# Performance work log

Hardware: AMD Instinct MI355X
Metric: run time of the kernel (lower is better)

The kernel has to match this reference:

```python
import jax, jax.numpy as jnp
import numpy as np

HIDDEN = 2048
HEADS = 16
KV_HEADS = 1
HEAD_DIM = 128
SEQ = 2048
BATCH = 1
LAM = 0.5


def _rotate_half(x):
    h = x.shape[-1] // 2
    return jnp.concatenate([-x[..., h:], x[..., :h]], axis=-1)


def _apply_rope(t, cos, sin):
    # t: [B,S,H,D], cos/sin: [S,D] -> broadcast over batch & heads
    c = cos[None, :, None, :]
    s = sin[None, :, None, :]
    return t * c + _rotate_half(t) * s


def setup_inputs() -> dict:
    key = jax.random.key(0)
    ks = jax.random.split(key, 8)
    x = jax.random.normal(ks[0], (BATCH, SEQ, HIDDEN), dtype=jnp.float32)
    # realistic RoPE tables, rotate-half layout: [S, D]
    inv_freq = 1.0 / (10000.0 ** (np.arange(0, HEAD_DIM, 2, dtype=np.float32) / HEAD_DIM))
    t = np.arange(SEQ, dtype=np.float32)
    ang = np.outer(t, inv_freq)                      # [S, D/2]
    ang = np.concatenate([ang, ang], axis=-1)        # [S, D]
    freqs_cos = jnp.asarray(np.cos(ang))
    freqs_sin = jnp.asarray(np.sin(ang))
    mask = jnp.tril(jnp.ones((SEQ, SEQ), dtype=bool))  # causal, True = attend
    scale = 1.0 / np.sqrt(HIDDEN)
    q1_w = jax.random.normal(ks[1], (HIDDEN, HEADS * HEAD_DIM), dtype=jnp.float32) * scale
    q2_w = jax.random.normal(ks[2], (HIDDEN, HEADS * HEAD_DIM), dtype=jnp.float32) * scale
    k_w = jax.random.normal(ks[3], (HIDDEN, KV_HEADS * HEAD_DIM), dtype=jnp.float32) * scale
    v_w = jax.random.normal(ks[4], (HIDDEN, KV_HEADS * HEAD_DIM), dtype=jnp.float32) * scale
    out_w = jax.random.normal(ks[5], (HEADS * HEAD_DIM, HIDDEN), dtype=jnp.float32) * scale
    return {"x": x, "freqs_cos": freqs_cos, "freqs_sin": freqs_sin, "mask": mask,
            "q1_w": q1_w, "q2_w": q2_w, "k_w": k_w, "v_w": v_w, "out_w": out_w}


def reference(x, freqs_cos, freqs_sin, mask, q1_w, q2_w, k_w, v_w, out_w):
    B, S, _ = x.shape
    q1 = (x @ q1_w).reshape(B, S, HEADS, HEAD_DIM)
    q2 = (x @ q2_w).reshape(B, S, HEADS, HEAD_DIM)
    k = (x @ k_w).reshape(B, S, KV_HEADS, HEAD_DIM)
    v = (x @ v_w).reshape(B, S, KV_HEADS, HEAD_DIM)
    q1 = _apply_rope(q1, freqs_cos, freqs_sin)
    q2 = _apply_rope(q2, freqs_cos, freqs_sin)
    k = _apply_rope(k, freqs_cos, freqs_sin)
    # MQA broadcast of the single KV head
    k = jnp.repeat(k, HEADS // KV_HEADS, axis=2)  # [B,S,H,D]
    v = jnp.repeat(v, HEADS // KV_HEADS, axis=2)
    inv_sqrt_d = 1.0 / jnp.sqrt(jnp.float32(HEAD_DIM))
    s1 = jnp.einsum('bqhd,bkhd->bhqk', q1, k) * inv_sqrt_d
    s2 = jnp.einsum('bqhd,bkhd->bhqk', q2, k) * inv_sqrt_d
    m = mask[None, None, :, :]
    neg = jnp.float32(-1e10)
    s1 = jnp.where(m, s1, neg)
    s2 = jnp.where(m, s2, neg)
    a1 = jax.nn.softmax(s1, axis=-1)
    a2 = jax.nn.softmax(s2, axis=-1)
    a = a1 - LAM * a2
    a = a / (jnp.sum(a, axis=-1, keepdims=True) + 1e-8)
    a = jnp.maximum(a, 0.0)
    out = jnp.einsum('bhqk,bkhd->bqhd', a, v).reshape(B, S, HEADS * HEAD_DIM)
    return out @ out_w
```

## Files before the change

### kernel.cpp

```cpp
#include <hip/hip_runtime.h>
#include <hip/hip_bf16.h>

typedef __attribute__((ext_vector_type(8))) short bf16x8;
typedef __attribute__((ext_vector_type(4))) float f32x4;

#define MFMA16(a, b, c) __builtin_amdgcn_mfma_f32_16x16x32_bf16((a), (b), (c), 0, 0, 0)

#define LDQ 4352
#define KSCALE 0.12751743f

__device__ __forceinline__ ushort f2bf(float f) {
    unsigned int x = __float_as_uint(f);
    x += 0x7fffu + ((x >> 16) & 1u);
    return (ushort)(x >> 16);
}
__device__ __forceinline__ float bf2f(ushort u) {
    return __uint_as_float(((unsigned int)u) << 16);
}
__device__ __forceinline__ float exp2_fast(float x) {
    float r;
    asm("v_exp_f32 %0, %1" : "=v"(r) : "v"(x));
    return r;
}
__device__ __forceinline__ unsigned int cvtpk(float lo, float hi) {
    unsigned int r;
    asm("v_cvt_pk_bf16_f32 %0, %1, %2" : "=v"(r) : "v"(lo), "v"(hi));
    return r;
}

__device__ __forceinline__ void gload16(const ushort* g, ushort* l) {
    __builtin_amdgcn_global_load_lds((const __attribute__((address_space(1))) unsigned int*)g,
                                     (__attribute__((address_space(3))) unsigned int*)l, 16, 0, 0);
}

__global__ __launch_bounds__(256) void prep_k(const float* __restrict__ x, ushort* __restrict__ xb,
                                              const float* __restrict__ q1w, const float* __restrict__ q2w,
                                              const float* __restrict__ kw, const float* __restrict__ vw,
                                              const float* __restrict__ ow,
                                              ushort* __restrict__ w1t, ushort* __restrict__ w2t,
                                              ushort* __restrict__ wkt, ushort* __restrict__ wvt,
                                              ushort* __restrict__ wot) {
    int bid = blockIdx.x;
    if (bid < 4096) {
        int i = bid * 256 + threadIdx.x;
        float4 v = ((const float4*)x)[i];
        ushort4 u;
        u.x = f2bf(v.x); u.y = f2bf(v.y); u.z = f2bf(v.z); u.w = f2bf(v.w);
        ((ushort4*)xb)[i] = u;
        return;
    }
    bid -= 4096;
    const float* in;
    ushort* out;
    int C, TX;
    if (bid < 4096) { in = q1w; out = w1t; C = 2048; TX = 64; }
    else if (bid < 8192) { bid -= 4096; in = q2w; out = w2t; C = 2048; TX = 64; }
    else if (bid < 12288) { bid -= 8192; in = ow; out = wot; C = 2048; TX = 64; }
    else if (bid < 12544) { bid -= 12288; in = kw; out = wkt; C = 128; TX = 4; }
    else { bid -= 12544; in = vw; out = wvt; C = 128; TX = 4; }
    __shared__ ushort t[32][33];
    const int c0 = (bid % TX) * 32, r0 = (bid / TX) * 32;
    const int lx = threadIdx.x & 31, ly = threadIdx.x >> 5;
#pragma unroll
    for (int i = 0; i < 4; ++i)
        t[ly + i * 8][lx] = f2bf(in[(size_t)(r0 + ly + i * 8) * C + c0 + lx]);
    __syncthreads();
#pragma unroll
    for (int i = 0; i < 4; ++i)
        out[(size_t)(c0 + ly + i * 8) * 2048 + r0 + lx] = t[lx][ly + i * 8];
}

template <bool FUSE>
__global__ __launch_bounds__(512) void gemm8_k(const ushort* __restrict__ A, int lda,
                                               const ushort* __restrict__ Bt, int ldb,
                                               void* __restrict__ C, int ldc,
                                               int K, int nbx, int ntile, int cbf,
                                               size_t cstride,
                                               const float* __restrict__ cs,
                                               const float* __restrict__ sn,
                                               ushort* __restrict__ vtb) {
    __shared__ ushort As[2 * 4096];
    __shared__ ushort Bs[2 * 4096];
    const int tid = threadIdx.x;
    const int lane = tid & 63, wid = tid >> 6;
    const int cpx = (int)gridDim.x >> 3;
    const int swz = ((int)blockIdx.x & 7) * cpx + ((int)blockIdx.x >> 3);
    const int kslice = swz / ntile;
    const int tile = swz - kslice * ntile;
    const int nt = tile / nbx;
    const int m0 = (tile - nt * nbx) * 128, n0 = nt * 128;
    const int wr = wid >> 2, wc = wid & 3;
    const int l15 = lane & 15, lhi = lane >> 4;

    const int srow = tid >> 2;
    const int scol = (((tid & 3) ^ ((srow >> 1) & 3)) << 3) + kslice * K;
    const ushort* gA = A + (size_t)(m0 + srow) * lda + scol;
    const ushort* gB = Bt + (size_t)(n0 + srow) * ldb + scol;
    ushort* lA = &As[wid * 512];
    ushort* lB = &Bs[wid * 512];

    f32x4 acc[4][2];
#pragma unroll
    for (int m = 0; m < 4; ++m)
#pragma unroll
        for (int n = 0; n < 2; ++n) acc[m][n] = (f32x4){0.f, 0.f, 0.f, 0.f};

    const int fcol = (lhi << 4) ^ (((l15 >> 1) & 3) << 4);

    gload16(gA, lA);
    gload16(gB, lB);
    __syncthreads();

    int cur = 0;
    for (int k0 = 0; k0 < K; k0 += 32) {
        if (k0 + 32 < K) {
            gload16(gA + k0 + 32, lA + (cur ^ 1) * 4096);
            gload16(gB + k0 + 32, lB + (cur ^ 1) * 4096);
        }
        const char* aB = (const char*)&As[cur * 4096];
        const char* bB = (const char*)&Bs[cur * 4096];
        bf16x8 af[4], bfr[2];
#pragma unroll
        for (int m = 0; m < 4; ++m)
            af[m] = *(const bf16x8*)(aB + (wr * 64 + m * 16 + l15) * 64 + fcol);
#pragma unroll
        for (int n = 0; n < 2; ++n)
            bfr[n] = *(const bf16x8*)(bB + (wc * 16 + n * 64 + l15) * 64 + fcol);
#pragma unroll
        for (int m = 0; m < 4; ++m)
#pragma unroll
            for (int n = 0; n < 2; ++n)
                acc[m][n] = MFMA16(af[m], bfr[n], acc[m][n]);
        __syncthreads();
        cur ^= 1;
    }

    if (FUSE) {
        if (nt == 33) {
#pragma unroll
            for (int m = 0; m < 4; ++m) {
                const int rb = m0 + wr * 64 + m * 16 + lhi * 4;
#pragma unroll
                for (int n = 0; n < 2; ++n) {
                    const int d = wc * 16 + n * 64 + l15;
                    uint2 w;
                    w.x = cvtpk(acc[m][n][0], acc[m][n][1]);
                    w.y = cvtpk(acc[m][n][2], acc[m][n][3]);
                    *(uint2*)(vtb + (size_t)d * 2048 + rb) = w;
                }
            }
        } else {
            const float scale = (nt == 32) ? KSCALE : 1.0f;
            ushort* out = (ushort*)C;
            const int d0 = wc * 16 + l15;
#pragma unroll
            for (int m = 0; m < 4; ++m) {
                const int rb = m0 + wr * 64 + m * 16 + lhi * 4;
#pragma unroll
                for (int r = 0; r < 4; ++r) {
                    const int row = rb + r;
                    float c0 = cs[row * 128 + d0], c1 = cs[row * 128 + d0 + 64];
                    float s0 = sn[row * 128 + d0], s1 = sn[row * 128 + d0 + 64];
                    float t0 = acc[m][0][r], t1 = acc[m][1][r];
                    out[(size_t)row * ldc + n0 + d0] = f2bf((t0 * c0 - t1 * s0) * scale);
                    out[(size_t)row * ldc + n0 + d0 + 64] = f2bf((t1 * c1 + t0 * s1) * scale);
                }
            }
        }
    } else {
        char* Cp = (char*)C + kslice * cstride;
#pragma unroll
        for (int m = 0; m < 4; ++m) {
            const int rb = m0 + wr * 64 + m * 16 + lhi * 4;
#pragma unroll
            for (int n = 0; n < 2; ++n) {
                const int col = n0 + wc * 16 + n * 64 + l15;
#pragma unroll
                for (int r = 0; r < 4; ++r) {
                    if (cbf)
                        ((ushort*)Cp)[(size_t)(rb + r) * ldc + col] = f2bf(acc[m][n][r]);
                    else
                        ((float*)Cp)[(size_t)(rb + r) * ldc + col] = acc[m][n][r];
                }
            }
        }
    }
}


__device__ __forceinline__ void stage_k_chunk(const ushort* __restrict__ kb, int kc,
                                              ushort* __restrict__ kbuf, int wid, int lane) {
#pragma unroll
    for (int u = 0; u < 2; ++u) {
        const int w = wid * 2 + u;
        const int row = w * 4 + (lane >> 4);
        const int colb = ((lane & 15) * 16) ^ ((row & 7) << 4);
        gload16(kb + (size_t)(kc + row) * LDQ + (colb >> 1), kbuf + w * 512);
    }
}

__device__ __forceinline__ void stage_v_chunk(const ushort* __restrict__ vtb, int kc,
                                              ushort* __restrict__ vbuf, int wid, int lane) {
#pragma unroll
    for (int u = 0; u < 2; ++u) {
        const int w = wid * 2 + u;
        const int rowd = w * 16 + (lane >> 2);
        const int colb = ((lane & 3) * 16) ^ (((rowd >> 1) & 3) << 4);
        gload16(vtb + (size_t)rowd * 2048 + kc + (colb >> 1), vbuf + w * 512);
    }
}

__device__ __forceinline__ void load_k_frags(const ushort* __restrict__ kbuf, int l15, int lhi,
                                             bf16x8 kf[2][4]) {
    const char* kB = (const char*)kbuf;
#pragma unroll
    for (int n2 = 0; n2 < 2; ++n2) {
        const int r = n2 * 16 + l15;
#pragma unroll
        for (int c = 0; c < 4; ++c)
            kf[n2][c] = *(const bf16x8*)(kB + r * 256 + ((lhi * 16 + c * 64) ^ ((r & 7) << 4)));
    }
}

template <bool MASKED>
__device__ __forceinline__ void sums_chunk(const ushort* __restrict__ kbuf, int kc,
                                           int l15, int lhi, int qrow,
                                           const bf16x8* q1f, const bf16x8* q2f,
                                           float& sum1, float& sum2) {
    bf16x8 kf[2][4];
    load_k_frags(kbuf, l15, lhi, kf);
    f32x4 s1[2], s2[2];
#pragma unroll
    for (int n2 = 0; n2 < 2; ++n2) {
        s1[n2] = (f32x4){0.f, 0.f, 0.f, 0.f};
        s2[n2] = (f32x4){0.f, 0.f, 0.f, 0.f};
#pragma unroll
        for (int c = 0; c < 4; ++c) {
            s1[n2] = MFMA16(kf[n2][c], q1f[c], s1[n2]);
            s2[n2] = MFMA16(kf[n2][c], q2f[c], s2[n2]);
        }
    }
    const int kbase = kc + lhi * 4;
#pragma unroll
    for (int n2 = 0; n2 < 2; ++n2)
#pragma unroll
        for (int r = 0; r < 4; ++r) {
            float e1 = exp2_fast(s1[n2][r]);
            float e2 = exp2_fast(s2[n2][r]);
            if (MASKED) {
                bool ok = (kbase + n2 * 16 + r) <= qrow;
                e1 = ok ? e1 : 0.f;
                e2 = ok ? e2 : 0.f;
            }
            sum1 += e1;
            sum2 += e2;
        }
}

__global__ __launch_bounds__(256) void attn_sums_k(const ushort* __restrict__ qkv,
                                                   float* __restrict__ sums) {
    __shared__ ushort Kbuf[2 * 4096];
    const int bid = blockIdx.x;
    const int strip = 127 - (bid >> 3);
    const int cs = (bid >> 2) & 1;
    const int hg = bid & 3;
    const int q0 = strip << 4;
    const int lane = threadIdx.x & 63, wid = threadIdx.x >> 6;
    const int h = hg * 4 + wid;
    const int l15 = lane & 15, lhi = lane >> 4;
    const int qrow = q0 + l15;
    const ushort* kb = qkv + 4096;

    bf16x8 q1f[4], q2f[4];
    {
        size_t base = (size_t)qrow * LDQ + h * 128 + lhi * 8;
#pragma unroll
        for (int c = 0; c < 4; ++c) {
            q1f[c] = *(const bf16x8*)(qkv + base + c * 32);
            q2f[c] = *(const bf16x8*)(qkv + base + 2048 + c * 32);
        }
    }

    const int nchunk = (strip >> 1) + 1;
    const int ndiag = nchunk - 1;
    const int nch = (nchunk - cs + 1) >> 1;

    float sum1 = 0.f, sum2 = 0.f;
    if (nch > 0) stage_k_chunk(kb, cs * 32, Kbuf, wid, lane);
    for (int i = 0; i < nch; ++i) {
        const int ch = cs + 2 * i, kc = ch << 5;
        if (i + 1 < nch) {
            stage_k_chunk(kb, kc + 64, Kbuf + ((i + 1) & 1) * 4096, wid, lane);
            asm volatile("s_waitcnt vmcnt(2)" ::: "memory");
        } else {
            asm volatile("s_waitcnt vmcnt(0)" ::: "memory");
        }
        __builtin_amdgcn_s_barrier();
        const ushort* kcur = Kbuf + (i & 1) * 4096;
        if (ch == ndiag)
            sums_chunk<true>(kcur, kc, l15, lhi, qrow, q1f, q2f, sum1, sum2);
        else
            sums_chunk<false>(kcur, kc, l15, lhi, qrow, q1f, q2f, sum1, sum2);
        __builtin_amdgcn_s_barrier();
    }

    sum1 += __shfl_xor(sum1, 16);
    sum1 += __shfl_xor(sum1, 32);
    sum2 += __shfl_xor(sum2, 16);
    sum2 += __shfl_xor(sum2, 32);

    if (lhi == 0) {
        sums[(size_t)((cs * 2 + 0) * 16 + h) * 2048 + qrow] = sum1;
        sums[(size_t)((cs * 2 + 1) * 16 + h) * 2048 + qrow] = sum2;
    }
}

template <bool MASKED>
__device__ __forceinline__ void pv_chunk(const ushort* __restrict__ kbuf, const ushort* __restrict__ vbuf,
                                         int kc, ushort* __restrict__ Pb,
                                         int l15, int lhi, int qrow,
                                         const bf16x8* q1f, const bf16x8* q2f,
                                         float c1, float c2, f32x4* o) {
    bf16x8 kf[2][4];
    load_k_frags(kbuf, l15, lhi, kf);
    bf16x8 vf[8];
    const char* vB = (const char*)vbuf;
#pragma unroll
    for (int dt = 0; dt < 8; ++dt) {
        const int d = dt * 16 + l15;
        vf[dt] = *(const bf16x8*)(vB + d * 64 + ((lhi * 16) ^ (((d >> 1) & 3) << 4)));
    }
    f32x4 s1[2], s2[2];
#pragma unroll
    for (int n2 = 0; n2 < 2; ++n2) {
        s1[n2] = (f32x4){0.f, 0.f, 0.f, 0.f};
        s2[n2] = (f32x4){0.f, 0.f, 0.f, 0.f};
#pragma unroll
        for (int c = 0; c < 4; ++c) {
            s1[n2] = MFMA16(kf[n2][c], q1f[c], s1[n2]);
            s2[n2] = MFMA16(kf[n2][c], q2f[c], s2[n2]);
        }
    }
    const int kbase = kc + lhi * 4;
#pragma unroll
    for (int n2 = 0; n2 < 2; ++n2) {
        float p[4];
#pragma unroll
        for (int r = 0; r < 4; ++r) {
            float e1 = exp2_fast(s1[n2][r]) * c1;
            float e2 = exp2_fast(s2[n2][r]) * c2;
            float pv = fmaxf(e1 - e2, 0.f);
            if (MASKED) pv = ((kbase + n2 * 16 + r) <= qrow) ? pv : 0.f;
            p[r] = pv;
        }
        uint2 w;
        w.x = cvtpk(p[0], p[1]);
        w.y = cvtpk(p[2], p[3]);
        *(uint2*)(Pb + l15 * 40 + n2 * 16 + lhi * 4) = w;
    }
    asm volatile("s_waitcnt lgkmcnt(0)" ::: "memory");
    bf16x8 pf = *(const bf16x8*)(Pb + l15 * 40 + lhi * 8);
#pragma unroll
    for (int dt = 0; dt < 8; ++dt)
        o[dt] = MFMA16(pf, vf[dt], o[dt]);
}

__global__ __launch_bounds__(256) void attn_pv_k(const ushort* __restrict__ qkv,
                                                 const ushort* __restrict__ vtb,
                                                 const float* __restrict__ sums,
                                                 ushort* __restrict__ op0,
                                                 ushort* __restrict__ op1) {
    __shared__ ushort Kbuf[2 * 4096];
    __shared__ ushort Vbuf[2 * 4096];
    __shared__ ushort P[4][16][40];
    const int bid = blockIdx.x;
    const int strip = 127 - (bid >> 3);
    const int cs = (bid >> 2) & 1;
    const int hg = bid & 3;
    const int q0 = strip << 4;
    const int lane = threadIdx.x & 63, wid = threadIdx.x >> 6;
    const int h = hg * 4 + wid;
    const int l15 = lane & 15, lhi = lane >> 4;
    const int qrow = q0 + l15;
    const ushort* kb = qkv + 4096;

    bf16x8 q1f[4], q2f[4];
    {
        size_t base = (size_t)qrow * LDQ + h * 128 + lhi * 8;
#pragma unroll
        for (int c = 0; c < 4; ++c) {
            q1f[c] = *(const bf16x8*)(qkv + base + c * 32);
            q2f[c] = *(const bf16x8*)(qkv + base + 2048 + c * 32);
        }
    }

    const float sum1 = sums[(size_t)(0 * 16 + h) * 2048 + qrow] + sums[(size_t)(2 * 16 + h) * 2048 + qrow];
    const float sum2 = sums[(size_t)(1 * 16 + h) * 2048 + qrow] + sums[(size_t)(3 * 16 + h) * 2048 + qrow];
    const float inv_denom = 1.0f / (0.5f + 1e-8f);
    const float c1 = inv_denom / sum1;
    const float c2 = 0.5f * inv_denom / sum2;

    f32x4 o[8];
#pragma unroll
    for (int dt = 0; dt < 8; ++dt) o[dt] = (f32x4){0.f, 0.f, 0.f, 0.f};

    const int nchunk = (strip >> 1) + 1;
    const int ndiag = nchunk - 1;
    const int nch = (nchunk - cs + 1) >> 1;

    if (nch > 0) {
        stage_k_chunk(kb, cs * 32, Kbuf, wid, lane);
        stage_v_chunk(vtb, cs * 32, Vbuf, wid, lane);
    }
    for (int i = 0; i < nch; ++i) {
        const int ch = cs + 2 * i, kc = ch << 5;
        if (i + 1 < nch) {
            stage_k_chunk(kb, kc + 64, Kbuf + ((i + 1) & 1) * 4096, wid, lane);
            stage_v_chunk(vtb, kc + 64, Vbuf + ((i + 1) & 1) * 4096, wid, lane);
            asm volatile("s_waitcnt vmcnt(4)" ::: "memory");
        } else {
            asm volatile("s_waitcnt vmcnt(0)" ::: "memory");
        }
        __builtin_amdgcn_s_barrier();
        const ushort* kcur = Kbuf + (i & 1) * 4096;
        const ushort* vcur = Vbuf + (i & 1) * 4096;
        ushort* Pb = &P[wid][0][0];
        if (ch == ndiag)
            pv_chunk<true>(kcur, vcur, kc, Pb, l15, lhi, qrow, q1f, q2f, c1, c2, o);
        else
            pv_chunk<false>(kcur, vcur, kc, Pb, l15, lhi, qrow, q1f, q2f, c1, c2, o);
        __builtin_amdgcn_s_barrier();
    }

    ushort* op = cs ? op1 : op0;
#pragma unroll
    for (int dt = 0; dt < 8; ++dt)
#pragma unroll
        for (int r = 0; r < 4; ++r)
            op[(size_t)(q0 + lhi * 4 + r) * 2048 + h * 128 + dt * 16 + l15] = f2bf(o[dt][r]);
}

__device__ __forceinline__ unsigned int addbf2(unsigned int a, unsigned int b) {
    float alo = bf2f((ushort)a), ahi = bf2f((ushort)(a >> 16));
    float blo = bf2f((ushort)b), bhi = bf2f((ushort)(b >> 16));
    return (unsigned int)f2bf(alo + blo) | ((unsigned int)f2bf(ahi + bhi) << 16);
}
__global__ void combine_k(const ushort* __restrict__ o0, const ushort* __restrict__ o1,
                          ushort* __restrict__ out, int n8) {
    int i = blockIdx.x * blockDim.x + threadIdx.x;
    if (i >= n8) return;
    uint4 a = ((const uint4*)o0)[i];
    uint4 b = ((const uint4*)o1)[i];
    uint4 c;
    c.x = addbf2(a.x, b.x);
    c.y = addbf2(a.y, b.y);
    c.z = addbf2(a.z, b.z);
    c.w = addbf2(a.w, b.w);
    ((uint4*)out)[i] = c;
}

__global__ void opadd_k(const ushort* __restrict__ p0, const ushort* __restrict__ p1,
                        float* __restrict__ out, int n8) {
    int i = blockIdx.x * blockDim.x + threadIdx.x;
    if (i >= n8) return;
    uint4 a = ((const uint4*)p0)[i];
    uint4 b = ((const uint4*)p1)[i];
    float4 r0, r1;
    r0.x = bf2f((ushort)a.x) + bf2f((ushort)b.x);
    r0.y = bf2f((ushort)(a.x >> 16)) + bf2f((ushort)(b.x >> 16));
    r0.z = bf2f((ushort)a.y) + bf2f((ushort)b.y);
    r0.w = bf2f((ushort)(a.y >> 16)) + bf2f((ushort)(b.y >> 16));
    r1.x = bf2f((ushort)a.z) + bf2f((ushort)b.z);
    r1.y = bf2f((ushort)(a.z >> 16)) + bf2f((ushort)(b.z >> 16));
    r1.z = bf2f((ushort)a.w) + bf2f((ushort)b.w);
    r1.w = bf2f((ushort)(a.w >> 16)) + bf2f((ushort)(b.w >> 16));
    ((float4*)out)[i * 2] = r0;
    ((float4*)out)[i * 2 + 1] = r1;
}

extern "C" void kernel_launch(void* const* d_in, const int* in_sizes, int n_in,
                              void* d_out, int out_size, void* d_ws, size_t ws_size,
                              hipStream_t stream) {
    const int S = 2048, HID = 2048;

    const float* x = (const float*)d_in[0];
    const float* fcos = (const float*)d_in[1];
    const float* fsin = (const float*)d_in[2];
    const float* q1w = (const float*)d_in[4];
    const float* q2w = (const float*)d_in[5];
    const float* kw = (const float*)d_in[6];
    const float* vw = (const float*)d_in[7];
    const float* ow = (const float*)d_in[8];

    ushort* xb = (ushort*)d_ws;
    ushort* btq = xb + (size_t)4194304;
    ushort* w1t = btq;
    ushort* w2t = btq + (size_t)2048 * 2048;
    ushort* wkt = btq + (size_t)4096 * 2048;
    ushort* wvt = btq + (size_t)4224 * 2048;
    ushort* wot = btq + (size_t)8912896;
    ushort* qkvb = wot + (size_t)4194304;
    ushort* vtb = qkvb + (size_t)8912896;
    float* sums = (float*)(vtb + (size_t)262144);
    ushort* opart0 = xb;
    ushort* opart1 = w1t;
    ushort* aob = w2t;

    prep_k<<<dim3(16896), dim3(256), 0, stream>>>(x, xb, q1w, q2w, kw, vw, ow,
                                                  w1t, w2t, wkt, wvt, wot);

    gemm8_k<true><<<dim3(544), dim3(512), 0, stream>>>(xb, HID, btq, HID, qkvb, LDQ, HID, 16, 544, 1,
                                                       0, fcos, fsin, vtb);

    attn_sums_k<<<dim3(1024), dim3(256), 0, stream>>>(qkvb, sums);

    attn_pv_k<<<dim3(1024), dim3(256), 0, stream>>>(qkvb, vtb, sums, opart0, opart1);

    combine_k<<<dim3(2048), dim3(256), 0, stream>>>(opart0, opart1, aob, S * HID / 8);

    gemm8_k<false><<<dim3(512), dim3(512), 0, stream>>>(aob, HID, wot, HID, xb, HID, 1024, 16, 256, 1,
                                                        (size_t)4194304 * 2, nullptr, nullptr, nullptr);

    opadd_k<<<dim3(2048), dim3(256), 0, stream>>>(xb, w1t, (float*)d_out, S * HID / 8);
}
```

Before: 181.0 us.

## Double GEMM K-step to 64 per stage with new LDS swizzle

```diff
diff --git a/kernel.cpp b/kernel.cpp
--- a/kernel.cpp
+++ b/kernel.cpp
@@ -79,8 +79,8 @@
                                                const float* __restrict__ cs,
                                                const float* __restrict__ sn,
                                                ushort* __restrict__ vtb) {
-    __shared__ ushort As[2 * 4096];
-    __shared__ ushort Bs[2 * 4096];
+    __shared__ ushort As[2 * 8192];
+    __shared__ ushort Bs[2 * 8192];
     const int tid = threadIdx.x;
     const int lane = tid & 63, wid = tid >> 6;
     const int cpx = (int)gridDim.x >> 3;
@@ -92,10 +92,12 @@
     const int wr = wid >> 2, wc = wid & 3;
     const int l15 = lane & 15, lhi = lane >> 4;
 
-    const int srow = tid >> 2;
-    const int scol = (((tid & 3) ^ ((srow >> 1) & 3)) << 3) + kslice * K;
-    const ushort* gA = A + (size_t)(m0 + srow) * lda + scol;
-    const ushort* gB = Bt + (size_t)(n0 + srow) * ldb + scol;
+    const int srow = wid * 8 + (lane >> 3);
+    const int scolel = (((lane & 7) ^ (lane >> 3)) << 3) + kslice * K;
+    const ushort* gA0 = A + (size_t)(m0 + srow) * lda + scolel;
+    const ushort* gA1 = A + (size_t)(m0 + 64 + srow) * lda + scolel;
+    const ushort* gB0 = Bt + (size_t)(n0 + srow) * ldb + scolel;
+    const ushort* gB1 = Bt + (size_t)(n0 + 64 + srow) * ldb + scolel;
     ushort* lA = &As[wid * 512];
     ushort* lB = &Bs[wid * 512];
 
@@ -105,32 +107,44 @@
 #pragma unroll
         for (int n = 0; n < 2; ++n) acc[m][n] = (f32x4){0.f, 0.f, 0.f, 0.f};
 
-    const int fcol = (lhi << 4) ^ (((l15 >> 1) & 3) << 4);
-
-    gload16(gA, lA);
-    gload16(gB, lB);
+    const int rsw = (l15 & 7) << 4;
+
+    const int NS = K >> 6;
+    gload16(gA0, lA);
+    gload16(gA1, lA + 4096);
+    gload16(gB0, lB);
+    gload16(gB1, lB + 4096);
     __syncthreads();
 
     int cur = 0;
-    for (int k0 = 0; k0 < K; k0 += 32) {
-        if (k0 + 32 < K) {
-            gload16(gA + k0 + 32, lA + (cur ^ 1) * 4096);
-            gload16(gB + k0 + 32, lB + (cur ^ 1) * 4096);
-        }
-        const char* aB = (const char*)&As[cur * 4096];
-        const char* bB = (const char*)&Bs[cur * 4096];
-        bf16x8 af[4], bfr[2];
-#pragma unroll
-        for (int m = 0; m < 4; ++m)
-            af[m] = *(const bf16x8*)(aB + (wr * 64 + m * 16 + l15) * 64 + fcol);
-#pragma unroll
-        for (int n = 0; n < 2; ++n)
-            bfr[n] = *(const bf16x8*)(bB + (wc * 16 + n * 64 + l15) * 64 + fcol);
-#pragma unroll
-        for (int m = 0; m < 4; ++m)
+    for (int s = 0; s < NS; ++s) {
+        if (s + 1 < NS) {
+            const size_t go = (size_t)(s + 1) << 6;
+            gload16(gA0 + go, lA + (cur ^ 1) * 8192);
+            gload16(gA1 + go, lA + (cur ^ 1) * 8192 + 4096);
+            gload16(gB0 + go, lB + (cur ^ 1) * 8192);
+            gload16(gB1 + go, lB + (cur ^ 1) * 8192 + 4096);
+        }
+        const char* aB = (const char*)&As[cur * 8192];
+        const char* bB = (const char*)&Bs[cur * 8192];
+        bf16x8 af[4][2], bfr[2][2];
+#pragma unroll
+        for (int kk = 0; kk < 2; ++kk) {
+            const int kb = (kk * 64 + lhi * 16);
+#pragma unroll
+            for (int m = 0; m < 4; ++m)
+                af[m][kk] = *(const bf16x8*)(aB + (wr * 64 + m * 16 + l15) * 128 + (kb ^ rsw));
 #pragma unroll
             for (int n = 0; n < 2; ++n)
-                acc[m][n] = MFMA16(af[m], bfr[n], acc[m][n]);
+                bfr[n][kk] = *(const bf16x8*)(bB + (wc * 16 + n * 64 + l15) * 128 + (kb ^ rsw));
+        }
+#pragma unroll
+        for (int kk = 0; kk < 2; ++kk)
+#pragma unroll
+            for (int m = 0; m < 4; ++m)
+#pragma unroll
+                for (int n = 0; n < 2; ++n)
+                    acc[m][n] = MFMA16(af[m][kk], bfr[n][kk], acc[m][n]);
         __syncthreads();
         cur ^= 1;
     }
```

After: 199.9 us. 10.5% more time.
